# Kernel tuning notes

Measured on AMD Instinct MI355X. Metric: run time of the kernel, lower is better.

## Reference

```python
import jax, jax.numpy as jnp
import numpy as np

ROWS, COLS = 10, 4
B, N = 65536, 16


def setup_inputs() -> dict:
    key = jax.random.key(0)
    kx, kc = jax.random.split(key)
    # 0.5 scale keeps trace(x^(rows+1))^cols finite in float32 (spectral radius ~2)
    x = jax.random.normal(kx, (B, N, N), dtype=jnp.float32) * 0.5
    # kaiming_normal_ on a 2D (rows, cols) tensor: std = sqrt(2 / fan_in), fan_in = cols
    coef = jax.random.normal(kc, (ROWS, COLS), dtype=jnp.float32) * np.float32(np.sqrt(2.0 / COLS))
    return {"x": x, "coef": coef}


def reference(x, coef):
    # x: [B, N, N]; coef: [rows, cols]
    rows, cols = coef.shape
    n = x.shape[-1] * x.shape[-2]  # numel per sample

    A0 = jnp.matmul(x, x)  # x^2, the first a_series entry

    def step(A, _):
        # original records trace(a_series[i]) = trace(x^(i+2)), then advances the power
        tr = jnp.trace(A, axis1=-2, axis2=-1)  # [B]
        return jnp.matmul(x, A), tr

    _, traces = jax.lax.scan(step, A0, None, length=rows)  # traces: [rows, B]
    t = traces.T  # [B, rows]

    jexp = jnp.arange(1, cols + 1, dtype=jnp.float32)  # j+1 exponents
    iexp = jnp.arange(rows, dtype=jnp.float32)
    # feature[b, i, j] = trace(x^(i+2))^(j+1) / n^(i+j+1)
    denom = jnp.float32(n) ** (iexp[:, None] + jexp[None, :])  # [rows, cols]
    feats = (t[:, :, None] ** jexp[None, None, :]) / denom  # [B, rows, cols]

    # terms = coef * feats, summed over (rows, cols) per sample -> [B]
    return jnp.einsum('rc,brc->b', coef, feats)
```

## Files before the change

kernel.cpp:

```cpp
#include <hip/hip_runtime.h>

typedef __fp16 f16x4 __attribute__((ext_vector_type(4)));
typedef __fp16 f16x2 __attribute__((ext_vector_type(2)));
typedef float f32x4 __attribute__((ext_vector_type(4)));

__device__ __forceinline__ f16x4 cat(f16x2 lo, f16x2 hi) {
    return __builtin_shufflevector(lo, hi, 0, 1, 2, 3);
}
__device__ __forceinline__ f16x2 u2h(unsigned v) {
    union { unsigned u; f16x2 h; } x; x.u = v; return x.h;
}

template <int CTRL>
__device__ __forceinline__ float dpp_add(float v) {
    int s = __builtin_amdgcn_update_dpp(0, __float_as_int(v), CTRL, 0xf, 0xf, true);
    return v + __int_as_float(s);
}

__global__ __launch_bounds__(256) void acoef_kernel(
    const float* __restrict__ x,
    const float* __restrict__ coef,
    float* __restrict__ out)
{
    const int lane = threadIdx.x & 63;
    const int wave = threadIdx.x >> 6;
    const int b = blockIdx.x * 4 + wave;
    const float* __restrict__ xb = x + (size_t)b * 256;

    const int n = lane & 15;
    const int q = lane >> 4;

    const float4 a = *(const float4*)(xb + n * 16 + 4 * q);
    f16x4 xA = cat(__builtin_amdgcn_cvt_pkrtz(a.x, a.y),
                   __builtin_amdgcn_cvt_pkrtz(a.z, a.w));

    float b0 = xb[(4 * q + 0) * 16 + n];
    float b1 = xb[(4 * q + 1) * 16 + n];
    float b2 = xb[(4 * q + 2) * 16 + n];
    float b3 = xb[(4 * q + 3) * 16 + n];
    f16x4 xB = cat(__builtin_amdgcn_cvt_pkrtz(b0, b1),
                   __builtin_amdgcn_cvt_pkrtz(b2, b3));

    const f32x4 zero = {0.f, 0.f, 0.f, 0.f};
    f32x4 acc = __builtin_amdgcn_mfma_f32_16x16x16f16(xA, xB, zero, 0, 0, 0);

    const bool diagsel = ((n >> 2) == q);

    f16x2 prpk[6];
    float trf = 0.0f;

    #pragma unroll
    for (int s = 0; s < 10; ++s) {
        float selA = (n & 1) ? acc[1] : acc[0];
        float selB = (n & 1) ? acc[3] : acc[2];
        float dv   = (n & 2) ? selB : selA;
        float tr   = diagsel ? dv : 0.0f;
        if (s & 1) prpk[s >> 1] = __builtin_amdgcn_cvt_pkrtz(trf, tr);
        else       trf = tr;

        if (s < 9) {
            f16x4 bf = cat(__builtin_amdgcn_cvt_pkrtz(acc[0], acc[1]),
                           __builtin_amdgcn_cvt_pkrtz(acc[2], acc[3]));
            acc = __builtin_amdgcn_mfma_f32_16x16x16f16(xA, bf, zero, 0, 0, 0);
        }
    }
    prpk[5] = u2h(0u);

    unsigned slo = (n == 0 ? 0x3C00u : 0u) | (n == 1 ? 0x3C000000u : 0u);
    unsigned shi = (n == 2 ? 0x3C00u : 0u) | (n == 3 ? 0x3C000000u : 0u);
    f16x4 selB = cat(u2h(slo), u2h(shi));
    f16x4 onesA = cat(u2h(0x3C003C00u), u2h(0x3C003C00u));

    float result = 0.0f;
    #pragma unroll
    for (int p = 0; p < 3; ++p) {
        f16x4 Ap = cat(prpk[2 * p], prpk[2 * p + 1]);
        f32x4 c1 = __builtin_amdgcn_mfma_f32_16x16x16f16(Ap, selB, zero, 0, 0, 0);
        f16x4 Bp = cat(__builtin_amdgcn_cvt_pkrtz(c1[0], c1[1]),
                       __builtin_amdgcn_cvt_pkrtz(c1[2], c1[3]));
        f32x4 c2 = __builtin_amdgcn_mfma_f32_16x16x16f16(onesA, Bp, zero, 0, 0, 0);
        float t = c2[0];

        int s = 4 * p + n;
        int idx = s > 9 ? 9 : s;
        const float4 c = *(const float4*)(coef + 4 * idx);
        float sv = t * 0x1p-8f;
        float h = fmaf(sv, c.w, c.z);
        h = fmaf(sv, h, c.y);
        h = fmaf(sv, h, c.x);
        float scl = __int_as_float((127 - 8 * s) << 23);
        result = fmaf(sv * h, scl, result);
    }

    result = dpp_add<0xB1>(result);
    result = dpp_add<0x4E>(result);
    if (lane == 0) out[b] = result;
}

extern "C" void kernel_launch(void* const* d_in, const int* in_sizes, int n_in,
                              void* d_out, int out_size, void* d_ws, size_t ws_size,
                              hipStream_t stream) {
    const float* x    = (const float*)d_in[0];
    const float* coef = (const float*)d_in[1];
    float* out        = (float*)d_out;
    const int B = in_sizes[0] / 256;
    acoef_kernel<<<dim3(B / 4), dim3(256), 0, stream>>>(x, coef, out);
}
```

Measured before the change: 99.42 us.

## Use persistent grid-stride waves with register prefetch of next matrix

Replaces one-wave-per-sample launch with a fixed grid of 2048 blocks where each wave loops over samples with a grid stride. The next sample's matrix is loaded into registers while the current one goes through its MFMA chain, and the coefficient loads and scale factors are hoisted out of the loop. The goal is to hide global load latency behind the serial MFMA dependency chain and to cut per-block launch overhead. The cost is higher register pressure under the 8-waves occupancy hint, plus a redundant reload of the last sample.

```diff
diff --git a/kernel.cpp b/kernel.cpp
--- a/kernel.cpp
+++ b/kernel.cpp
@@ -10,91 +10,103 @@
 __device__ __forceinline__ f16x2 u2h(unsigned v) {
     union { unsigned u; f16x2 h; } x; x.u = v; return x.h;
 }
-
 template <int CTRL>
 __device__ __forceinline__ float dpp_add(float v) {
     int s = __builtin_amdgcn_update_dpp(0, __float_as_int(v), CTRL, 0xf, 0xf, true);
     return v + __int_as_float(s);
 }
 
-__global__ __launch_bounds__(256) void acoef_kernel(
+__global__ __launch_bounds__(256, 8) void acoef_kernel(
     const float* __restrict__ x,
     const float* __restrict__ coef,
-    float* __restrict__ out)
+    float* __restrict__ out,
+    int B)
 {
     const int lane = threadIdx.x & 63;
-    const int wave = threadIdx.x >> 6;
-    const int b = blockIdx.x * 4 + wave;
-    const float* __restrict__ xb = x + (size_t)b * 256;
+    const int wid  = (blockIdx.x * 256 + threadIdx.x) >> 6;
+    const int stride = gridDim.x * 4;
 
     const int n = lane & 15;
     const int q = lane >> 4;
-
-    const float4 a = *(const float4*)(xb + n * 16 + 4 * q);
-    f16x4 xA = cat(__builtin_amdgcn_cvt_pkrtz(a.x, a.y),
-                   __builtin_amdgcn_cvt_pkrtz(a.z, a.w));
-
-    float b0 = xb[(4 * q + 0) * 16 + n];
-    float b1 = xb[(4 * q + 1) * 16 + n];
-    float b2 = xb[(4 * q + 2) * 16 + n];
-    float b3 = xb[(4 * q + 3) * 16 + n];
-    f16x4 xB = cat(__builtin_amdgcn_cvt_pkrtz(b0, b1),
-                   __builtin_amdgcn_cvt_pkrtz(b2, b3));
-
-    const f32x4 zero = {0.f, 0.f, 0.f, 0.f};
-    f32x4 acc = __builtin_amdgcn_mfma_f32_16x16x16f16(xA, xB, zero, 0, 0, 0);
-
     const bool diagsel = ((n >> 2) == q);
-
-    f16x2 prpk[6];
-    float trf = 0.0f;
-
-    #pragma unroll
-    for (int s = 0; s < 10; ++s) {
-        float selA = (n & 1) ? acc[1] : acc[0];
-        float selB = (n & 1) ? acc[3] : acc[2];
-        float dv   = (n & 2) ? selB : selA;
-        float tr   = diagsel ? dv : 0.0f;
-        if (s & 1) prpk[s >> 1] = __builtin_amdgcn_cvt_pkrtz(trf, tr);
-        else       trf = tr;
-
-        if (s < 9) {
-            f16x4 bf = cat(__builtin_amdgcn_cvt_pkrtz(acc[0], acc[1]),
-                           __builtin_amdgcn_cvt_pkrtz(acc[2], acc[3]));
-            acc = __builtin_amdgcn_mfma_f32_16x16x16f16(xA, bf, zero, 0, 0, 0);
-        }
-    }
-    prpk[5] = u2h(0u);
 
     unsigned slo = (n == 0 ? 0x3C00u : 0u) | (n == 1 ? 0x3C000000u : 0u);
     unsigned shi = (n == 2 ? 0x3C00u : 0u) | (n == 3 ? 0x3C000000u : 0u);
-    f16x4 selB = cat(u2h(slo), u2h(shi));
-    f16x4 onesA = cat(u2h(0x3C003C00u), u2h(0x3C003C00u));
-
-    float result = 0.0f;
+    const f16x4 selB  = cat(u2h(slo), u2h(shi));
+    const f16x4 onesA = cat(u2h(0x3C003C00u), u2h(0x3C003C00u));
+    const f32x4 zero  = {0.f, 0.f, 0.f, 0.f};
+    float4 cf[3]; float scl[3];
     #pragma unroll
     for (int p = 0; p < 3; ++p) {
-        f16x4 Ap = cat(prpk[2 * p], prpk[2 * p + 1]);
-        f32x4 c1 = __builtin_amdgcn_mfma_f32_16x16x16f16(Ap, selB, zero, 0, 0, 0);
-        f16x4 Bp = cat(__builtin_amdgcn_cvt_pkrtz(c1[0], c1[1]),
-                       __builtin_amdgcn_cvt_pkrtz(c1[2], c1[3]));
-        f32x4 c2 = __builtin_amdgcn_mfma_f32_16x16x16f16(onesA, Bp, zero, 0, 0, 0);
-        float t = c2[0];
-
         int s = 4 * p + n;
         int idx = s > 9 ? 9 : s;
-        const float4 c = *(const float4*)(coef + 4 * idx);
-        float sv = t * 0x1p-8f;
-        float h = fmaf(sv, c.w, c.z);
-        h = fmaf(sv, h, c.y);
-        h = fmaf(sv, h, c.x);
-        float scl = __int_as_float((127 - 8 * s) << 23);
-        result = fmaf(sv * h, scl, result);
+        cf[p]  = *(const float4*)(coef + 4 * idx);
+        scl[p] = __int_as_float((127 - 8 * s) << 23);
     }
 
-    result = dpp_add<0xB1>(result);
-    result = dpp_add<0x4E>(result);
-    if (lane == 0) out[b] = result;
+    const int aoff = n * 16 + 4 * q;
+    const int boff = 4 * q * 16 + n;
+
+    int s = wid;
+    const float* xb = x + (size_t)s * 256;
+    float4 a = *(const float4*)(xb + aoff);
+    float b0 = xb[boff], b1 = xb[boff + 16], b2 = xb[boff + 32], b3 = xb[boff + 48];
+
+    while (true) {
+        const int s2 = s + stride;
+        const bool more = (s2 < B);
+        const float* xn = x + (size_t)(more ? s2 : s) * 256;
+        float4 an = *(const float4*)(xn + aoff);
+        float bn0 = xn[boff], bn1 = xn[boff + 16], bn2 = xn[boff + 32], bn3 = xn[boff + 48];
+
+        f16x4 xA = cat(__builtin_amdgcn_cvt_pkrtz(a.x, a.y),
+                       __builtin_amdgcn_cvt_pkrtz(a.z, a.w));
+        f16x4 xB = cat(__builtin_amdgcn_cvt_pkrtz(b0, b1),
+                       __builtin_amdgcn_cvt_pkrtz(b2, b3));
+
+        f32x4 acc = __builtin_amdgcn_mfma_f32_16x16x16f16(xA, xB, zero, 0, 0, 0);
+
+        f16x2 prpk[6];
+        float trf = 0.0f;
+        #pragma unroll
+        for (int st = 0; st < 10; ++st) {
+            float selA = (n & 1) ? acc[1] : acc[0];
+            float selBv = (n & 1) ? acc[3] : acc[2];
+            float dv = (n & 2) ? selBv : selA;
+            float tr = diagsel ? dv : 0.0f;
+            if (st & 1) prpk[st >> 1] = __builtin_amdgcn_cvt_pkrtz(trf, tr);
+            else        trf = tr;
+
+            if (st < 9) {
+                f16x4 bf = cat(__builtin_amdgcn_cvt_pkrtz(acc[0], acc[1]),
+                               __builtin_amdgcn_cvt_pkrtz(acc[2], acc[3]));
+                acc = __builtin_amdgcn_mfma_f32_16x16x16f16(xA, bf, zero, 0, 0, 0);
+            }
+        }
+        prpk[5] = u2h(0u);
+
+        float result = 0.0f;
+        #pragma unroll
+        for (int p = 0; p < 3; ++p) {
+            f16x4 Ap = cat(prpk[2 * p], prpk[2 * p + 1]);
+            f32x4 c1 = __builtin_amdgcn_mfma_f32_16x16x16f16(Ap, selB, zero, 0, 0, 0);
+            f16x4 Bp = cat(__builtin_amdgcn_cvt_pkrtz(c1[0], c1[1]),
+                           __builtin_amdgcn_cvt_pkrtz(c1[2], c1[3]));
+            f32x4 c2 = __builtin_amdgcn_mfma_f32_16x16x16f16(onesA, Bp, zero, 0, 0, 0);
+            float t = c2[0];
+            float sv = t * 0x1p-8f;
+            float h = fmaf(sv, cf[p].w, cf[p].z);
+            h = fmaf(sv, h, cf[p].y);
+            h = fmaf(sv, h, cf[p].x);
+            result = fmaf(sv * h, scl[p], result);
+        }
+        result = dpp_add<0xB1>(result);
+        result = dpp_add<0x4E>(result);
+        if (lane == 0) out[s] = result;
+
+        if (!more) break;
+        s = s2; a = an; b0 = bn0; b1 = bn1; b2 = bn2; b3 = bn3;
+    }
 }
 
 extern "C" void kernel_launch(void* const* d_in, const int* in_sizes, int n_in,
@@ -104,5 +116,5 @@
     const float* coef = (const float*)d_in[1];
     float* out        = (float*)d_out;
     const int B = in_sizes[0] / 256;
-    acoef_kernel<<<dim3(B / 4), dim3(256), 0, stream>>>(x, coef, out);
+    acoef_kernel<<<dim3(2048), dim3(256), 0, stream>>>(x, coef, out, B);
 }
```

After: 96.12 us. -3.3%, faster.
